# Kernel optimization log

Hardware: AMD Instinct MI355X
Metric: run time of the kernel (lower is better)

The kernel has to match this reference:

```python
import jax, jax.numpy as jnp
import numpy as np

B, T, I, H, L = 64, 512, 512, 1024, 2

def _gru_layer(x, w_ih, w_hh, b_ih, b_hh):
    # x: [B,T,In]; w_ih: [3H,In]; w_hh: [3H,H]; biases: [3H]; gate order r,z,n (PyTorch)
    xg = jnp.einsum('bti,gi->btg', x, w_ih) + b_ih  # [B,T,3H] precomputed input gates
    h0 = jnp.zeros((x.shape[0], w_hh.shape[1]), x.dtype)
    w_hh_T = w_hh.T  # [H,3H]
    def step(h, xg_t):
        hg = h @ w_hh_T + b_hh                      # [B,3H]
        xr, xz, xn = jnp.split(xg_t, 3, axis=-1)
        hr, hz, hn = jnp.split(hg, 3, axis=-1)
        r = jax.nn.sigmoid(xr + hr)
        z = jax.nn.sigmoid(xz + hz)
        n = jnp.tanh(xn + r * hn)
        h_new = (1.0 - z) * n + z * h
        return h_new, h_new
    _, Hs = jax.lax.scan(step, h0, jnp.swapaxes(xg, 0, 1))  # [T,B,H]
    return jnp.swapaxes(Hs, 0, 1)                           # [B,T,H]

def setup_inputs() -> dict:
    key = jax.random.key(0)
    ks = jax.random.split(key, 1 + 4 * L)
    x = jax.random.normal(ks[0], (B, T, I), dtype=jnp.float32)
    s = 1.0 / np.sqrt(H)
    inp = {"x": x}
    for l in range(L):
        in_dim = I if l == 0 else H
        k0, k1, k2, k3 = ks[1 + 4 * l: 5 + 4 * l]
        inp[f"w_ih_{l}"] = jax.random.uniform(k0, (3 * H, in_dim), jnp.float32, -s, s)
        inp[f"w_hh_{l}"] = jax.random.uniform(k1, (3 * H, H), jnp.float32, -s, s)
        inp[f"b_ih_{l}"] = jax.random.uniform(k2, (3 * H,), jnp.float32, -s, s)
        inp[f"b_hh_{l}"] = jax.random.uniform(k3, (3 * H,), jnp.float32, -s, s)
    return inp

def reference(x, w_ih_0, w_hh_0, b_ih_0, b_hh_0, w_ih_1, w_hh_1, b_ih_1, b_hh_1):
    h = _gru_layer(x, w_ih_0, w_hh_0, b_ih_0, b_hh_0)
    h = _gru_layer(h, w_ih_1, w_hh_1, b_ih_1, b_hh_1)
    return h[:, -1, :]  # [B,H] last timestep (unidirectional)
```

## Files before the change

### kernel.cpp

```cpp
#include <hip/hip_runtime.h>
#include <cmath>

#define B_  64
#define T_  512
#define I_  512
#define H_  1024
#define TI_ (T_ * I_)
#define TH_ (T_ * H_)
#define CK  64
#define CP  65
#define NBLK 256
#define NTHR 256

__device__ __forceinline__ void bar_arrive(unsigned* ctr)
{
  __syncthreads();
  if (threadIdx.x == 0)
    __hip_atomic_fetch_add(ctr, 1u, __ATOMIC_RELEASE, __HIP_MEMORY_SCOPE_AGENT);
}

__device__ __forceinline__ void bar_wait(unsigned* ctr, unsigned target)
{
  if (threadIdx.x == 0) {
    while (__hip_atomic_load(ctr, __ATOMIC_RELAXED, __HIP_MEMORY_SCOPE_AGENT) < target)
      __builtin_amdgcn_s_sleep(1);
    (void)__hip_atomic_load(ctr, __ATOMIC_ACQUIRE, __HIP_MEMORY_SCOPE_AGENT);
  }
  __syncthreads();
}

__device__ __forceinline__ void chunk_fma(const float* cb, int b,
                                          const float* wr, const float* wz, const float* wn,
                                          float& aR, float& aZ, float& aN)
{
#pragma unroll
  for (int k4 = 0; k4 < CK / 4; ++k4) {
    float4 WR = *(const float4*)(wr + k4 * 4);
    float4 WZ = *(const float4*)(wz + k4 * 4);
    float4 WN = *(const float4*)(wn + k4 * 4);
    float v0 = cb[(k4 * 4 + 0) * CP + b];
    float v1 = cb[(k4 * 4 + 1) * CP + b];
    float v2 = cb[(k4 * 4 + 2) * CP + b];
    float v3 = cb[(k4 * 4 + 3) * CP + b];
    aR = fmaf(WR.x, v0, aR); aZ = fmaf(WZ.x, v0, aZ); aN = fmaf(WN.x, v0, aN);
    aR = fmaf(WR.y, v1, aR); aZ = fmaf(WZ.y, v1, aZ); aN = fmaf(WN.y, v1, aN);
    aR = fmaf(WR.z, v2, aR); aZ = fmaf(WZ.z, v2, aZ); aN = fmaf(WN.z, v2, aN);
    aR = fmaf(WR.w, v3, aR); aZ = fmaf(WZ.w, v3, aZ); aN = fmaf(WN.w, v3, aN);
  }
}

__device__ __forceinline__ void stage_store(float* cbw, int q4, int r0,
                                            const float4& pf0, const float4& pf1,
                                            const float4& pf2, const float4& pf3)
{
  cbw[(q4 + 0) * CP + (r0 +  0)] = pf0.x;
  cbw[(q4 + 1) * CP + (r0 +  0)] = pf0.y;
  cbw[(q4 + 2) * CP + (r0 +  0)] = pf0.z;
  cbw[(q4 + 3) * CP + (r0 +  0)] = pf0.w;
  cbw[(q4 + 0) * CP + (r0 + 16)] = pf1.x;
  cbw[(q4 + 1) * CP + (r0 + 16)] = pf1.y;
  cbw[(q4 + 2) * CP + (r0 + 16)] = pf1.z;
  cbw[(q4 + 3) * CP + (r0 + 16)] = pf1.w;
  cbw[(q4 + 0) * CP + (r0 + 32)] = pf2.x;
  cbw[(q4 + 1) * CP + (r0 + 32)] = pf2.y;
  cbw[(q4 + 2) * CP + (r0 + 32)] = pf2.z;
  cbw[(q4 + 3) * CP + (r0 + 32)] = pf2.w;
  cbw[(q4 + 0) * CP + (r0 + 48)] = pf3.x;
  cbw[(q4 + 1) * CP + (r0 + 48)] = pf3.y;
  cbw[(q4 + 2) * CP + (r0 + 48)] = pf3.z;
  cbw[(q4 + 3) * CP + (r0 + 48)] = pf3.w;
}

__device__ __forceinline__ void phase_chunks(float (*chunk)[CK * CP], int nchunks,
                                             const float* src, size_t pitch,
                                             const float* wr, const float* wz, const float* wn,
                                             float& aR, float& aZ, float& aN,
                                             int q4, int r0, int b)
{
  float4 pf0, pf1, pf2, pf3;
  {
    const float* p = src + q4;
    pf0 = *(const float4*)(p + (size_t)(r0 +  0) * pitch);
    pf1 = *(const float4*)(p + (size_t)(r0 + 16) * pitch);
    pf2 = *(const float4*)(p + (size_t)(r0 + 32) * pitch);
    pf3 = *(const float4*)(p + (size_t)(r0 + 48) * pitch);
  }
  for (int c = 0; c < nchunks; ++c) {
    stage_store(chunk[c & 1], q4, r0, pf0, pf1, pf2, pf3);
    if (c + 1 < nchunks) {
      const float* p = src + (c + 1) * CK + q4;
      pf0 = *(const float4*)(p + (size_t)(r0 +  0) * pitch);
      pf1 = *(const float4*)(p + (size_t)(r0 + 16) * pitch);
      pf2 = *(const float4*)(p + (size_t)(r0 + 32) * pitch);
      pf3 = *(const float4*)(p + (size_t)(r0 + 48) * pitch);
    }
    __syncthreads();
    chunk_fma(chunk[c & 1], b, wr + c * CK, wz + c * CK, wn + c * CK, aR, aZ, aN);
  }
}

__global__ void __launch_bounds__(NTHR)
gru_fused(const float* __restrict__ x,
          const float* __restrict__ wih0, const float* __restrict__ whh0,
          const float* __restrict__ bih0, const float* __restrict__ bhh0,
          const float* __restrict__ wih1, const float* __restrict__ whh1,
          const float* __restrict__ bih1, const float* __restrict__ bhh1,
          float* __restrict__ h1, float* __restrict__ hb0, float* __restrict__ hb1,
          unsigned* __restrict__ bar, float* __restrict__ out)
{
  __shared__ float chunk[2][CK * CP];

  const int tid = threadIdx.x;
  const int b   = tid & 63;
  const int jj  = __builtin_amdgcn_readfirstlane(tid >> 6);
  const int j   = blockIdx.x * 4 + jj;
  const int q4  = (tid & 15) * 4;
  const int r0  = tid >> 4;

  for (int layer = 0; layer < 2; ++layer) {
    const int Ki  = layer ? H_ : I_;
    const int NCX = Ki / CK;
    const int NCH = H_ / CK;

    const float* wih = layer ? wih1 : wih0;
    const float* whh = layer ? whh1 : whh0;
    const float* bih = layer ? bih1 : bih0;
    const float* bhh = layer ? bhh1 : bhh0;

    const float* wxr = wih + (size_t)(0 * H_ + j) * Ki;
    const float* wxz = wih + (size_t)(1 * H_ + j) * Ki;
    const float* wxn = wih + (size_t)(2 * H_ + j) * Ki;
    const float* whr = whh + (size_t)(0 * H_ + j) * H_;
    const float* whz = whh + (size_t)(1 * H_ + j) * H_;
    const float* whn = whh + (size_t)(2 * H_ + j) * H_;

    const float bR  = bih[j] + bhh[j];
    const float bZ  = bih[H_ + j] + bhh[H_ + j];
    const float bXN = bih[2 * H_ + j];
    const float bHN = bhh[2 * H_ + j];

    float hreg = 0.0f;

    for (int t = 0; t < T_; ++t) {
      float accR = bR, accZ = bZ, accXN = bXN, accHN = bHN;

      if (layer == 1 && t == 0) bar_wait(bar, (unsigned)T_ * NBLK);

      const float* xsrc = layer ? (h1 + (size_t)t * H_) : (x + (size_t)t * I_);
      const size_t xpit = layer ? (size_t)TH_ : (size_t)TI_;
      phase_chunks(chunk, NCX, xsrc, xpit, wxr, wxz, wxn,
                   accR, accZ, accXN, q4, r0, b);

      if (t > 0) {
        bar_wait(bar, (unsigned)(layer * T_ + t) * NBLK);
        const float* hsrc = layer ? ((t & 1) ? hb0 : hb1)
                                  : (h1 + (size_t)(t - 1) * H_);
        const size_t hpit = layer ? (size_t)H_ : (size_t)TH_;
        phase_chunks(chunk, NCH, hsrc, hpit, whr, whz, whn,
                     accR, accZ, accHN, q4, r0, b);
      }

      const float r = 1.0f / (1.0f + expf(-accR));
      const float z = 1.0f / (1.0f + expf(-accZ));
      const float n = tanhf(accXN + r * accHN);
      const float hnew = (1.0f - z) * n + z * hreg;
      hreg = hnew;

      if (layer == 0) {
        h1[(size_t)b * TH_ + (size_t)t * H_ + j] = hnew;
      } else {
        ((t & 1) ? hb1 : hb0)[b * H_ + j] = hnew;
        if (t == T_ - 1) out[b * H_ + j] = hnew;
      }

      if (!(layer == 1 && t == T_ - 1))
        bar_arrive(bar);
    }
  }
}

extern "C" void kernel_launch(void* const* d_in, const int* in_sizes, int n_in,
                              void* d_out, int out_size, void* d_ws, size_t ws_size,
                              hipStream_t stream)
{
  const float* x    = (const float*)d_in[0];
  const float* wih0 = (const float*)d_in[1];
  const float* whh0 = (const float*)d_in[2];
  const float* bih0 = (const float*)d_in[3];
  const float* bhh0 = (const float*)d_in[4];
  const float* wih1 = (const float*)d_in[5];
  const float* whh1 = (const float*)d_in[6];
  const float* bih1 = (const float*)d_in[7];
  const float* bhh1 = (const float*)d_in[8];
  float* out = (float*)d_out;

  float* h1  = (float*)d_ws;
  float* hb0 = h1 + (size_t)B_ * T_ * H_;
  float* hb1 = hb0 + (size_t)B_ * H_;
  unsigned* bar = (unsigned*)(hb1 + (size_t)B_ * H_);

  hipMemsetAsync(bar, 0, 256, stream);

  void* args[] = { (void*)&x,
                   (void*)&wih0, (void*)&whh0, (void*)&bih0, (void*)&bhh0,
                   (void*)&wih1, (void*)&whh1, (void*)&bih1, (void*)&bhh1,
                   (void*)&h1, (void*)&hb0, (void*)&hb1, (void*)&bar, (void*)&out };

  hipLaunchCooperativeKernel((const void*)gru_fused,
                             dim3(NBLK), dim3(NTHR), args, 0, stream);
}
```

Before: 48.03 ms.

## Replace atomic counter grid barrier with per-block flags and coherent loads

Replaces the single atomic-add counter barrier with per-block sequence flags that each block publishes with a release store. All 256 threads poll the flags in parallel, and the acquire fence is dropped in the per-step wait. To keep the recurrent hidden-state reads correct without the acquire, those loads become relaxed agent-scope atomic scalar loads instead of float4 loads. The aim is to cut atomic contention on one counter at every timestep, at the cost of scalarized hidden-state loads and weaker ordering guarantees.

Result: slower. 53.42 ms (+11.2%).

```diff
diff --git a/kernel.cpp b/kernel.cpp
--- a/kernel.cpp
+++ b/kernel.cpp
@@ -12,21 +12,37 @@
 #define NBLK 256
 #define NTHR 256
 
-__device__ __forceinline__ void bar_arrive(unsigned* ctr)
+__device__ __forceinline__ float ldcg(const float* p)
+{
+  return __hip_atomic_load(p, __ATOMIC_RELAXED, __HIP_MEMORY_SCOPE_AGENT);
+}
+__device__ __forceinline__ float4 ldcg4(const float* p)
+{
+  float4 v;
+  v.x = ldcg(p + 0); v.y = ldcg(p + 1); v.z = ldcg(p + 2); v.w = ldcg(p + 3);
+  return v;
+}
+
+__device__ __forceinline__ void publish(unsigned* flags, int bid, unsigned seq)
 {
   __syncthreads();
   if (threadIdx.x == 0)
-    __hip_atomic_fetch_add(ctr, 1u, __ATOMIC_RELEASE, __HIP_MEMORY_SCOPE_AGENT);
-}
-
-__device__ __forceinline__ void bar_wait(unsigned* ctr, unsigned target)
-{
-  if (threadIdx.x == 0) {
-    while (__hip_atomic_load(ctr, __ATOMIC_RELAXED, __HIP_MEMORY_SCOPE_AGENT) < target)
+    __hip_atomic_store(&flags[bid], seq, __ATOMIC_RELEASE, __HIP_MEMORY_SCOPE_AGENT);
+}
+
+__device__ __forceinline__ void waitall(unsigned* flags, unsigned target, bool acq)
+{
+  const int tid = threadIdx.x;
+  if (tid < NBLK) {
+    while (__hip_atomic_load(&flags[tid], __ATOMIC_RELAXED, __HIP_MEMORY_SCOPE_AGENT) < target)
       __builtin_amdgcn_s_sleep(1);
-    (void)__hip_atomic_load(ctr, __ATOMIC_ACQUIRE, __HIP_MEMORY_SCOPE_AGENT);
   }
   __syncthreads();
+  if (acq) {
+    if (tid == 0)
+      (void)__hip_atomic_load(&flags[0], __ATOMIC_ACQUIRE, __HIP_MEMORY_SCOPE_AGENT);
+    __syncthreads();
+  }
 }
 
 __device__ __forceinline__ void chunk_fma(const float* cb, int b,
@@ -71,28 +87,34 @@
   cbw[(q4 + 3) * CP + (r0 + 48)] = pf3.w;
 }
 
+template <bool COH>
 __device__ __forceinline__ void phase_chunks(float (*chunk)[CK * CP], int nchunks,
                                              const float* src, size_t pitch,
                                              const float* wr, const float* wz, const float* wn,
                                              float& aR, float& aZ, float& aN,
                                              int q4, int r0, int b)
 {
+  auto LD4 = [](const float* p) -> float4 {
+    if constexpr (COH) return ldcg4(p);
+    else               return *(const float4*)p;
+  };
+
   float4 pf0, pf1, pf2, pf3;
   {
     const float* p = src + q4;
-    pf0 = *(const float4*)(p + (size_t)(r0 +  0) * pitch);
-    pf1 = *(const float4*)(p + (size_t)(r0 + 16) * pitch);
-    pf2 = *(const float4*)(p + (size_t)(r0 + 32) * pitch);
-    pf3 = *(const float4*)(p + (size_t)(r0 + 48) * pitch);
+    pf0 = LD4(p + (size_t)(r0 +  0) * pitch);
+    pf1 = LD4(p + (size_t)(r0 + 16) * pitch);
+    pf2 = LD4(p + (size_t)(r0 + 32) * pitch);
+    pf3 = LD4(p + (size_t)(r0 + 48) * pitch);
   }
   for (int c = 0; c < nchunks; ++c) {
     stage_store(chunk[c & 1], q4, r0, pf0, pf1, pf2, pf3);
     if (c + 1 < nchunks) {
       const float* p = src + (c + 1) * CK + q4;
-      pf0 = *(const float4*)(p + (size_t)(r0 +  0) * pitch);
-      pf1 = *(const float4*)(p + (size_t)(r0 + 16) * pitch);
-      pf2 = *(const float4*)(p + (size_t)(r0 + 32) * pitch);
-      pf3 = *(const float4*)(p + (size_t)(r0 + 48) * pitch);
+      pf0 = LD4(p + (size_t)(r0 +  0) * pitch);
+      pf1 = LD4(p + (size_t)(r0 + 16) * pitch);
+      pf2 = LD4(p + (size_t)(r0 + 32) * pitch);
+      pf3 = LD4(p + (size_t)(r0 + 48) * pitch);
     }
     __syncthreads();
     chunk_fma(chunk[c & 1], b, wr + c * CK, wz + c * CK, wn + c * CK, aR, aZ, aN);
@@ -106,14 +128,15 @@
           const float* __restrict__ wih1, const float* __restrict__ whh1,
           const float* __restrict__ bih1, const float* __restrict__ bhh1,
           float* __restrict__ h1, float* __restrict__ hb0, float* __restrict__ hb1,
-          unsigned* __restrict__ bar, float* __restrict__ out)
+          unsigned* __restrict__ flags, float* __restrict__ out)
 {
   __shared__ float chunk[2][CK * CP];
 
   const int tid = threadIdx.x;
   const int b   = tid & 63;
   const int jj  = __builtin_amdgcn_readfirstlane(tid >> 6);
-  const int j   = blockIdx.x * 4 + jj;
+  const int bid = blockIdx.x;
+  const int j   = bid * 4 + jj;
   const int q4  = (tid & 15) * 4;
   const int r0  = tid >> 4;
 
@@ -144,20 +167,20 @@
     for (int t = 0; t < T_; ++t) {
       float accR = bR, accZ = bZ, accXN = bXN, accHN = bHN;
 
-      if (layer == 1 && t == 0) bar_wait(bar, (unsigned)T_ * NBLK);
+      if (layer == 1 && t == 0) waitall(flags, (unsigned)T_, true);
 
       const float* xsrc = layer ? (h1 + (size_t)t * H_) : (x + (size_t)t * I_);
       const size_t xpit = layer ? (size_t)TH_ : (size_t)TI_;
-      phase_chunks(chunk, NCX, xsrc, xpit, wxr, wxz, wxn,
-                   accR, accZ, accXN, q4, r0, b);
+      phase_chunks<false>(chunk, NCX, xsrc, xpit, wxr, wxz, wxn,
+                          accR, accZ, accXN, q4, r0, b);
 
       if (t > 0) {
-        bar_wait(bar, (unsigned)(layer * T_ + t) * NBLK);
+        waitall(flags, (unsigned)(layer * T_ + t), false);
         const float* hsrc = layer ? ((t & 1) ? hb0 : hb1)
                                   : (h1 + (size_t)(t - 1) * H_);
         const size_t hpit = layer ? (size_t)H_ : (size_t)TH_;
-        phase_chunks(chunk, NCH, hsrc, hpit, whr, whz, whn,
-                     accR, accZ, accHN, q4, r0, b);
+        phase_chunks<true>(chunk, NCH, hsrc, hpit, whr, whz, whn,
+                           accR, accZ, accHN, q4, r0, b);
       }
 
       const float r = 1.0f / (1.0f + expf(-accR));
@@ -174,7 +197,7 @@
       }
 
       if (!(layer == 1 && t == T_ - 1))
-        bar_arrive(bar);
+        publish(flags, bid, (unsigned)(layer * T_ + t + 1));
     }
   }
 }
@@ -197,14 +220,14 @@
   float* h1  = (float*)d_ws;
   float* hb0 = h1 + (size_t)B_ * T_ * H_;
   float* hb1 = hb0 + (size_t)B_ * H_;
-  unsigned* bar = (unsigned*)(hb1 + (size_t)B_ * H_);
-
-  hipMemsetAsync(bar, 0, 256, stream);
+  unsigned* flags = (unsigned*)(hb1 + (size_t)B_ * H_);
+
+  hipMemsetAsync(flags, 0, NBLK * sizeof(unsigned), stream);
 
   void* args[] = { (void*)&x,
                    (void*)&wih0, (void*)&whh0, (void*)&bih0, (void*)&bhh0,
                    (void*)&wih1, (void*)&whh1, (void*)&bih1, (void*)&bhh1,
-                   (void*)&h1, (void*)&hb0, (void*)&hb1, (void*)&bar, (void*)&out };
+                   (void*)&h1, (void*)&hb0, (void*)&hb1, (void*)&flags, (void*)&out };
 
   hipLaunchCooperativeKernel((const void*)gru_fused,
                              dim3(NBLK), dim3(NTHR), args, 0, stream);
```
